# Kernel tuning notes

Measured on AMD Instinct MI355X. Metric: run time of the kernel, lower is better.

## Reference

```python
import jax, jax.numpy as jnp
import numpy as np

N, E, D, H, O = 50000, 1_600_000, 128, 64, 128
BN_EPS = 1e-5


def setup_inputs() -> dict:
    key = jax.random.key(0)
    ks = jax.random.split(key, 8)
    feat = jax.random.normal(ks[0], (N, D), dtype=jnp.float32)
    src = jax.random.randint(ks[1], (E,), 0, N, dtype=jnp.int32)
    dst = jax.random.randint(ks[2], (E,), 0, N, dtype=jnp.int32)
    s = 1.0 / np.sqrt(D)
    gamma = jnp.ones((D,), jnp.float32)
    beta = jnp.zeros((D,), jnp.float32)
    Wq = (jax.random.normal(ks[3], (D, H), dtype=jnp.float32) * s)
    bq = jnp.zeros((H,), jnp.float32)
    Wk = (jax.random.normal(ks[4], (D, H), dtype=jnp.float32) * s)
    Wv = (jax.random.normal(ks[5], (D, O), dtype=jnp.float32) * s)
    we = (jax.random.normal(ks[6], (H,), dtype=jnp.float32) / np.sqrt(H))
    return {"feat": feat, "gamma": gamma, "beta": beta, "Wq": Wq, "bq": bq,
            "Wk": Wk, "Wv": Wv, "we": we, "src": src, "dst": dst}


def reference(feat, gamma, beta, Wq, bq, Wk, Wv, we, src, dst):
    n = feat.shape[0]
    # BatchNorm1d (training-style: batch mean, biased variance)
    mean = feat.mean(axis=0)
    var = feat.var(axis=0)
    x = (feat - mean) * jax.lax.rsqrt(var + BN_EPS) * gamma + beta
    # node projections
    q = x @ Wq + bq          # [N, H]
    k = x @ Wk               # [N, H]
    v = x @ Wv               # [N, O]
    # u_add_v + fc_e(sigmoid(.)): per-edge score  [E]
    e = jax.nn.sigmoid(q[src] + k[dst]) @ we
    # edge_softmax grouped by destination node
    m = jax.ops.segment_max(e, dst, num_segments=n)
    ex = jnp.exp(e - m[dst])
    denom = jax.ops.segment_sum(ex, dst, num_segments=n)
    a = ex / denom[dst]      # [E]
    # u_mul_e_sum: weighted scatter-sum aggregation  [N, O]
    rst = jax.ops.segment_sum(v[src] * a[:, None], dst, num_segments=n)
    return rst
```

## Files before the change

### kernel.cpp

```cpp
#include <hip/hip_runtime.h>
#include <hip/hip_bf16.h>
#include <math.h>

#define BN_EPS 1e-5f
#define PGRID 256
#define CAP 96
#define CAPB 9216

typedef unsigned int u32;
typedef unsigned short u16;
typedef __attribute__((ext_vector_type(8))) short short8;
typedef __attribute__((ext_vector_type(4))) float floatx4;

__device__ __forceinline__ float bf_lo(u32 u) { return __uint_as_float(u << 16); }
__device__ __forceinline__ float bf_hi(u32 u) { return __uint_as_float(u & 0xffff0000u); }
__device__ __forceinline__ u32 bfpair(float lo, float hi) {
  u32 a = __float_as_uint(lo); a += 0x7fffu + ((a >> 16) & 1);
  u32 b = __float_as_uint(hi); b += 0x7fffu + ((b >> 16) & 1);
  return (a >> 16) | (b & 0xffff0000u);
}
__device__ __forceinline__ float sigm(float x) {
  return __builtin_amdgcn_rcpf(1.f + __expf(-x));
}

__global__ __launch_bounds__(256) void k1_stats_part_pack(
    const float* __restrict__ feat, float* __restrict__ colsum, float* __restrict__ colsq, long total,
    const int* __restrict__ src, const int* __restrict__ dst,
    int* __restrict__ bcur, u32* __restrict__ pbuf, int E, int epb, int nbuck,
    const float* __restrict__ Wq, const float* __restrict__ Wk, const float* __restrict__ Wv,
    u32* __restrict__ wt) {
  int tid = threadIdx.x;
  int bid = blockIdx.x;
  if (bid < 256) {
    long g0 = (long)bid * 256 + tid;
    float s = 0.f, sq = 0.f;
    for (long g = g0; g < total; g += 65536) { float x = feat[g]; s += x; sq += x * x; }
    __shared__ float ls[256], lq[256];
    ls[tid] = s; lq[tid] = sq;
    __syncthreads();
    if (tid < 128) {
      atomicAdd(&colsum[tid], ls[tid] + ls[tid + 128]);
      atomicAdd(&colsq[tid],  lq[tid] + lq[tid + 128]);
    }
  } else if (bid < 256 + PGRID) {
    int p = bid - 256;
    int lo = p * epb;
    int hi = lo + epb; if (hi > E) hi = E;
    __shared__ int bc_l[256], gb_l[256], cur_l[256];
    bc_l[tid] = 0;
    __syncthreads();
    for (int i = lo + tid; i < hi; i += 256)
      atomicAdd(&bc_l[dst[i] >> 8], 1);
    __syncthreads();
    if (tid < nbuck && bc_l[tid] > 0) gb_l[tid] = atomicAdd(&bcur[tid], bc_l[tid]);
    cur_l[tid] = 0;
    __syncthreads();
    for (int i = lo + tid; i < hi; i += 256) {
      int d = dst[i], s = src[i];
      int b = d >> 8;
      int r = gb_l[b] + atomicAdd(&cur_l[b], 1);
      if (r < CAPB) pbuf[(size_t)b * CAPB + r] = ((u32)(d & 255) << 16) | (u32)s;
    }
  } else {
    int col = tid;
    for (int dp = 0; dp < 64; ++dp) {
      int d = dp * 2;
      float lo, hi;
      if (col < 64)       { lo = Wq[d * 64 + col];        hi = Wq[(d + 1) * 64 + col]; }
      else if (col < 128) { lo = Wk[d * 64 + col - 64];   hi = Wk[(d + 1) * 64 + col - 64]; }
      else                { lo = Wv[d * 128 + col - 128]; hi = Wv[(d + 1) * 128 + col - 128]; }
      u32 byte = (u32)col * 256 + (u32)d * 2;
      byte ^= (u32)(col & 7) << 4;
      wt[byte >> 2] = bfpair(lo, hi);
    }
  }
}

__global__ __launch_bounds__(256) void k2_qkv_group(
    const float* __restrict__ feat, const float* __restrict__ colsum, const float* __restrict__ colsq,
    const float* __restrict__ gamma, const float* __restrict__ beta, const float* __restrict__ bq,
    const u32* __restrict__ wt,
    __hip_bfloat16* __restrict__ qbuf, float* __restrict__ kbuf, __hip_bfloat16* __restrict__ vbuf,
    int N, float invN, int QBn,
    const int* __restrict__ bcur, const u32* __restrict__ pbuf,
    int* __restrict__ cnt, u16* __restrict__ esrc) {
  int tid = threadIdx.x;
  __shared__ u32 wlds[16384];
  __shared__ float sc_lds[128], sh_lds[128];
  if ((int)blockIdx.x >= QBn) {
    int b = (int)blockIdx.x - QBn;
    int nbase = b * 256;
    int* hcur = (int*)wlds;
    hcur[tid] = 0;
    __syncthreads();
    int bc = bcur[b]; if (bc > CAPB) bc = CAPB;
    const u32* pb = pbuf + (size_t)b * CAPB;
    for (int i = tid; i < bc; i += 256) {
      u32 e = pb[i];
      int d = e >> 16, s = e & 0xffff;
      int r = atomicAdd(&hcur[d], 1);
      if (r < CAP) esrc[(size_t)(nbase + d) * CAP + r] = (u16)s;
    }
    __syncthreads();
    int nid = nbase + tid;
    if (nid < N) cnt[nid] = hcur[tid];
    return;
  }
  {
    const uint4* wg = (const uint4*)wt;
    uint4* wl = (uint4*)wlds;
#pragma unroll
    for (int i = 0; i < 16; ++i) wl[tid + i * 256] = wg[tid + i * 256];
  }
  if (tid < 128) {
    float mean = colsum[tid] * invN;
    float var  = colsq[tid] * invN - mean * mean;
    float inv  = rsqrtf(var + BN_EPS);
    float s    = gamma[tid] * inv;
    sc_lds[tid] = s; sh_lds[tid] = beta[tid] - mean * s;
  }
  __syncthreads();
  int lane = tid & 63, wv = tid >> 6;
  int arow = blockIdx.x * 64 + wv * 16 + (lane & 15);
  int kb16 = lane >> 4;
  const float* frow = feat + (long)(arow < N ? arow : N - 1) * 128;
  u32 afr[4][4];
#pragma unroll
  for (int kk = 0; kk < 4; ++kk) {
    int d0 = kk * 32 + kb16 * 8;
    float4 x0 = *(const float4*)(frow + d0);
    float4 x1 = *(const float4*)(frow + d0 + 4);
    float4 s0 = *(const float4*)&sc_lds[d0];
    float4 s1 = *(const float4*)&sc_lds[d0 + 4];
    float4 h0 = *(const float4*)&sh_lds[d0];
    float4 h1 = *(const float4*)&sh_lds[d0 + 4];
    float n0 = fmaf(x0.x, s0.x, h0.x), n1 = fmaf(x0.y, s0.y, h0.y);
    float n2 = fmaf(x0.z, s0.z, h0.z), n3 = fmaf(x0.w, s0.w, h0.w);
    float n4 = fmaf(x1.x, s1.x, h1.x), n5 = fmaf(x1.y, s1.y, h1.y);
    float n6 = fmaf(x1.z, s1.z, h1.z), n7 = fmaf(x1.w, s1.w, h1.w);
    afr[kk][0] = bfpair(n0, n1); afr[kk][1] = bfpair(n2, n3);
    afr[kk][2] = bfpair(n4, n5); afr[kk][3] = bfpair(n6, n7);
  }
  floatx4 acc[16];
#pragma unroll
  for (int ct = 0; ct < 16; ++ct) acc[ct] = (floatx4){0.f, 0.f, 0.f, 0.f};
#pragma unroll
  for (int kk = 0; kk < 4; ++kk) {
    union { u32 u[4]; short8 s; } au;
    au.u[0] = afr[kk][0]; au.u[1] = afr[kk][1]; au.u[2] = afr[kk][2]; au.u[3] = afr[kk][3];
#pragma unroll
    for (int ct = 0; ct < 16; ++ct) {
      int col = ct * 16 + (lane & 15);
      u32 byte = ((u32)col * 256 + (u32)(kk * 64 + kb16 * 16)) ^ ((u32)(col & 7) << 4);
      union { uint4 u4; short8 s; } bu;
      bu.u4 = *(const uint4*)((const char*)wlds + byte);
      acc[ct] = __builtin_amdgcn_mfma_f32_16x16x32_bf16(au.s, bu.s, acc[ct], 0, 0, 0);
    }
  }
  int crow0 = blockIdx.x * 64 + wv * 16 + (lane >> 4) * 4;
#pragma unroll
  for (int ct = 0; ct < 16; ++ct) {
    int col = ct * 16 + (lane & 15);
    float bqc = (ct < 4) ? bq[col] : 0.f;
#pragma unroll
    for (int i = 0; i < 4; ++i) {
      int row = crow0 + i;
      if (row < N) {
        float val = acc[ct][i];
        if (ct < 4)      qbuf[row * 64 + col] = __float2bfloat16(val + bqc);
        else if (ct < 8) kbuf[row * 64 + col - 64] = val;
        else             vbuf[row * 128 + col - 128] = __float2bfloat16(val);
      }
    }
  }
}

__global__ __launch_bounds__(256) void node_kernel(
    const __hip_bfloat16* __restrict__ qbt, const float* __restrict__ kb,
    const __hip_bfloat16* __restrict__ vbt, const float* __restrict__ we,
    const int* __restrict__ cnt, const u16* __restrict__ esrc,
    float* __restrict__ out, int N) {
  int tid = threadIdx.x;
  int lane = tid & 63, wvi = tid >> 6;
  int n = blockIdx.x * 4 + wvi;
  if (n >= N) return;
  int g8 = lane >> 3, hq = lane & 7;
  int deg = cnt[n]; if (deg > CAP) deg = CAP;
  int base = n * CAP;
  const uint4* qb4 = (const uint4*)qbt;
  const u32* vb32 = (const u32*)vbt;
  float4 ka  = ((const float4*)(kb + n * 64))[hq * 2];
  float4 kc  = ((const float4*)(kb + n * 64))[hq * 2 + 1];
  float4 wa  = ((const float4*)we)[hq * 2];
  float4 wb  = ((const float4*)we)[hq * 2 + 1];
  float dsum = 0.f, ax = 0.f, ay = 0.f;
  int sreg = (lane < deg) ? (int)esrc[base + lane] : 0;
  for (int cs = 0; cs < deg; cs += 64) {
    int cn = deg - cs; if (cn > 64) cn = 64;
    int rem = deg - cs - 64;
    int snext = (rem > 0 && lane < rem) ? (int)esrc[base + cs + 64 + lane] : 0;
    int nr = (cn + 7) >> 3;
    int sj0 = __shfl(sreg, g8, 64);
    uint4 qv = qb4[sj0 * 8 + hq];
    for (int r = 0; r < nr; ++r) {
      uint4 qnext;
      if (r + 1 < nr) {
        int sjn = __shfl(sreg, (r + 1) * 8 + g8, 64);
        qnext = qb4[sjn * 8 + hq];
      }
      float p;
      p  = wa.x * sigm(bf_lo(qv.x) + ka.x);
      p += wa.y * sigm(bf_hi(qv.x) + ka.y);
      p += wa.z * sigm(bf_lo(qv.y) + ka.z);
      p += wa.w * sigm(bf_hi(qv.y) + ka.w);
      p += wb.x * sigm(bf_lo(qv.z) + kc.x);
      p += wb.y * sigm(bf_hi(qv.z) + kc.y);
      p += wb.z * sigm(bf_lo(qv.w) + kc.z);
      p += wb.w * sigm(bf_hi(qv.w) + kc.w);
      p += __shfl_xor(p, 1, 64);
      p += __shfl_xor(p, 2, 64);
      p += __shfl_xor(p, 4, 64);
      int eidx = r * 8 + g8;
      float wgt = (eidx < cn) ? __expf(p) : 0.f;
      dsum += wgt;
#pragma unroll
      for (int jj = 0; jj < 8; ++jj) {
        float wj = __shfl(wgt, jj * 8, 64);
        int s2 = __shfl(sreg, r * 8 + jj, 64);
        u32 vp = vb32[s2 * 64 + lane];
        ax = fmaf(wj, bf_lo(vp), ax);
        ay = fmaf(wj, bf_hi(vp), ay);
      }
      if (r + 1 < nr) qv = qnext;
    }
    sreg = snext;
  }
  dsum += __shfl_xor(dsum, 8, 64);
  dsum += __shfl_xor(dsum, 16, 64);
  dsum += __shfl_xor(dsum, 32, 64);
  float2 r = make_float2(0.f, 0.f);
  if (deg > 0) {
    float iv = __builtin_amdgcn_rcpf(dsum);
    r.x = ax * iv; r.y = ay * iv;
  }
  ((float2*)out)[n * 64 + lane] = r;
}

extern "C" void kernel_launch(void* const* d_in, const int* in_sizes, int n_in,
                              void* d_out, int out_size, void* d_ws, size_t ws_size,
                              hipStream_t stream) {
  const float* feat  = (const float*)d_in[0];
  const float* gamma = (const float*)d_in[1];
  const float* beta  = (const float*)d_in[2];
  const float* Wq    = (const float*)d_in[3];
  const float* bq    = (const float*)d_in[4];
  const float* Wk    = (const float*)d_in[5];
  const float* Wv    = (const float*)d_in[6];
  const float* we    = (const float*)d_in[7];
  const int*   src   = (const int*)d_in[8];
  const int*   dst   = (const int*)d_in[9];
  float* out = (float*)d_out;

  const int N  = in_sizes[0] / 128;
  const int E  = in_sizes[8];
  const int QB = (N + 63) / 64;
  const int NBUCK = (N + 255) / 256;
  const int EPB = (E + PGRID - 1) / PGRID;

  char* ws = (char*)d_ws;
  size_t off = 0;
  auto alloc = [&](size_t bytes) { char* p = ws + off; off = (off + bytes + 511) & ~(size_t)511; return p; };
  float* colsum = (float*)alloc(128 * 4);
  float* colsq  = (float*)alloc(128 * 4);
  int*   bcur   = (int*)alloc((size_t)NBUCK * 4);
  u32*   wt     = (u32*)alloc(16384 * 4);
  __hip_bfloat16* qb = (__hip_bfloat16*)alloc((size_t)N * 64 * 2);
  float*          kb = (float*)alloc((size_t)N * 64 * 4);
  __hip_bfloat16* vb = (__hip_bfloat16*)alloc((size_t)N * 128 * 2);
  int* cnt  = (int*)alloc((size_t)N * 4);
  u16* esrc = (u16*)alloc((size_t)N * CAP * 2);
  u32* pbuf = (u32*)alloc((size_t)NBUCK * CAPB * 4);

  hipMemsetAsync(colsum, 0, 1024, stream);
  hipMemsetAsync(bcur, 0, (size_t)NBUCK * 4, stream);

  k1_stats_part_pack<<<256 + PGRID + 1, 256, 0, stream>>>(
      feat, colsum, colsq, (long)N * 128, src, dst, bcur, pbuf, E, EPB, NBUCK, Wq, Wk, Wv, wt);
  k2_qkv_group<<<QB + NBUCK, 256, 0, stream>>>(
      feat, colsum, colsq, gamma, beta, bq, wt, qb, kb, vb, N, 1.0f / (float)N, QB,
      bcur, pbuf, cnt, esrc);
  node_kernel<<<(N + 3) / 4, 256, 0, stream>>>(qb, kb, vb, we, cnt, esrc, out, N);
}
```

Before: 153.5 us.

## Widen partition grid, split weight packing, prescale by log2e, vectorize V gather

Doubles the edge-partition grid and spreads weight packing across 16 blocks instead of one serial block. Q and K are prescaled by log2(e) so the sigmoid uses exp2 directly. The V aggregation now loads uint2 per lane, handling two edges per half-wave, and combines the halves with a final shuffle before a float4 store. The two memsets are merged into one. Together these aim to cut a serial tail, transcendental work and memory instruction count, at the cost of some extra shuffles and slightly different bf16 rounding of the scaled Q.

```diff
diff --git a/kernel.cpp b/kernel.cpp
--- a/kernel.cpp
+++ b/kernel.cpp
@@ -3,9 +3,11 @@
 #include <math.h>
 
 #define BN_EPS 1e-5f
-#define PGRID 256
+#define PGRID 512
+#define WPACK 16
 #define CAP 96
 #define CAPB 9216
+#define LOG2E 1.4426950408889634f
 
 typedef unsigned int u32;
 typedef unsigned short u16;
@@ -19,8 +21,8 @@
   u32 b = __float_as_uint(hi); b += 0x7fffu + ((b >> 16) & 1);
   return (a >> 16) | (b & 0xffff0000u);
 }
-__device__ __forceinline__ float sigm(float x) {
-  return __builtin_amdgcn_rcpf(1.f + __expf(-x));
+__device__ __forceinline__ float sigm2(float xs) {
+  return __builtin_amdgcn_rcpf(1.f + exp2f(-xs));
 }
 
 __global__ __launch_bounds__(256) void k1_stats_part_pack(
@@ -62,8 +64,9 @@
       if (r < CAPB) pbuf[(size_t)b * CAPB + r] = ((u32)(d & 255) << 16) | (u32)s;
     }
   } else {
+    int wb = bid - (256 + PGRID);
     int col = tid;
-    for (int dp = 0; dp < 64; ++dp) {
+    for (int dp = wb * 4; dp < wb * 4 + 4; ++dp) {
       int d = dp * 2;
       float lo, hi;
       if (col < 64)       { lo = Wq[d * 64 + col];        hi = Wq[(d + 1) * 64 + col]; }
@@ -167,8 +170,8 @@
       int row = crow0 + i;
       if (row < N) {
         float val = acc[ct][i];
-        if (ct < 4)      qbuf[row * 64 + col] = __float2bfloat16(val + bqc);
-        else if (ct < 8) kbuf[row * 64 + col - 64] = val;
+        if (ct < 4)      qbuf[row * 64 + col] = __float2bfloat16((val + bqc) * LOG2E);
+        else if (ct < 8) kbuf[row * 64 + col - 64] = val * LOG2E;
         else             vbuf[row * 128 + col - 128] = __float2bfloat16(val);
       }
     }
@@ -185,15 +188,17 @@
   int n = blockIdx.x * 4 + wvi;
   if (n >= N) return;
   int g8 = lane >> 3, hq = lane & 7;
+  int l32 = lane & 31, ehalf = lane >> 5;
   int deg = cnt[n]; if (deg > CAP) deg = CAP;
   int base = n * CAP;
   const uint4* qb4 = (const uint4*)qbt;
-  const u32* vb32 = (const u32*)vbt;
+  const uint2* vb2 = (const uint2*)vbt;
   float4 ka  = ((const float4*)(kb + n * 64))[hq * 2];
   float4 kc  = ((const float4*)(kb + n * 64))[hq * 2 + 1];
   float4 wa  = ((const float4*)we)[hq * 2];
   float4 wb  = ((const float4*)we)[hq * 2 + 1];
-  float dsum = 0.f, ax = 0.f, ay = 0.f;
+  float dsum = 0.f;
+  float a0 = 0.f, a1 = 0.f, a2 = 0.f, a3 = 0.f;
   int sreg = (lane < deg) ? (int)esrc[base + lane] : 0;
   for (int cs = 0; cs < deg; cs += 64) {
     int cn = deg - cs; if (cn > 64) cn = 64;
@@ -209,27 +214,30 @@
         qnext = qb4[sjn * 8 + hq];
       }
       float p;
-      p  = wa.x * sigm(bf_lo(qv.x) + ka.x);
-      p += wa.y * sigm(bf_hi(qv.x) + ka.y);
-      p += wa.z * sigm(bf_lo(qv.y) + ka.z);
-      p += wa.w * sigm(bf_hi(qv.y) + ka.w);
-      p += wb.x * sigm(bf_lo(qv.z) + kc.x);
-      p += wb.y * sigm(bf_hi(qv.z) + kc.y);
-      p += wb.z * sigm(bf_lo(qv.w) + kc.z);
-      p += wb.w * sigm(bf_hi(qv.w) + kc.w);
+      p  = wa.x * sigm2(bf_lo(qv.x) + ka.x);
+      p += wa.y * sigm2(bf_hi(qv.x) + ka.y);
+      p += wa.z * sigm2(bf_lo(qv.y) + ka.z);
+      p += wa.w * sigm2(bf_hi(qv.y) + ka.w);
+      p += wb.x * sigm2(bf_lo(qv.z) + kc.x);
+      p += wb.y * sigm2(bf_hi(qv.z) + kc.y);
+      p += wb.z * sigm2(bf_lo(qv.w) + kc.z);
+      p += wb.w * sigm2(bf_hi(qv.w) + kc.w);
       p += __shfl_xor(p, 1, 64);
       p += __shfl_xor(p, 2, 64);
       p += __shfl_xor(p, 4, 64);
       int eidx = r * 8 + g8;
-      float wgt = (eidx < cn) ? __expf(p) : 0.f;
+      float wgt = (eidx < cn) ? exp2f(p * LOG2E) : 0.f;
       dsum += wgt;
 #pragma unroll
-      for (int jj = 0; jj < 8; ++jj) {
-        float wj = __shfl(wgt, jj * 8, 64);
-        int s2 = __shfl(sreg, r * 8 + jj, 64);
-        u32 vp = vb32[s2 * 64 + lane];
-        ax = fmaf(wj, bf_lo(vp), ax);
-        ay = fmaf(wj, bf_hi(vp), ay);
+      for (int pp = 0; pp < 4; ++pp) {
+        int le = pp * 2 + ehalf;
+        float wj = __shfl(wgt, le * 8, 64);
+        int s2   = __shfl(sreg, r * 8 + le, 64);
+        uint2 vp = vb2[s2 * 32 + l32];
+        a0 = fmaf(wj, bf_lo(vp.x), a0);
+        a1 = fmaf(wj, bf_hi(vp.x), a1);
+        a2 = fmaf(wj, bf_lo(vp.y), a2);
+        a3 = fmaf(wj, bf_hi(vp.y), a3);
       }
       if (r + 1 < nr) qv = qnext;
     }
@@ -238,12 +246,18 @@
   dsum += __shfl_xor(dsum, 8, 64);
   dsum += __shfl_xor(dsum, 16, 64);
   dsum += __shfl_xor(dsum, 32, 64);
-  float2 r = make_float2(0.f, 0.f);
-  if (deg > 0) {
-    float iv = __builtin_amdgcn_rcpf(dsum);
-    r.x = ax * iv; r.y = ay * iv;
-  }
-  ((float2*)out)[n * 64 + lane] = r;
+  a0 += __shfl_xor(a0, 32, 64);
+  a1 += __shfl_xor(a1, 32, 64);
+  a2 += __shfl_xor(a2, 32, 64);
+  a3 += __shfl_xor(a3, 32, 64);
+  if (lane < 32) {
+    float4 o = make_float4(0.f, 0.f, 0.f, 0.f);
+    if (deg > 0) {
+      float iv = __builtin_amdgcn_rcpf(dsum);
+      o = make_float4(a0 * iv, a1 * iv, a2 * iv, a3 * iv);
+    }
+    ((float4*)out)[n * 32 + l32] = o;
+  }
 }
 
 extern "C" void kernel_launch(void* const* d_in, const int* in_sizes, int n_in,
@@ -270,9 +284,9 @@
   char* ws = (char*)d_ws;
   size_t off = 0;
   auto alloc = [&](size_t bytes) { char* p = ws + off; off = (off + bytes + 511) & ~(size_t)511; return p; };
-  float* colsum = (float*)alloc(128 * 4);
-  float* colsq  = (float*)alloc(128 * 4);
-  int*   bcur   = (int*)alloc((size_t)NBUCK * 4);
+  float* colsum = (float*)alloc(2048);
+  float* colsq  = colsum + 128;
+  int*   bcur   = (int*)(colsum + 256);
   u32*   wt     = (u32*)alloc(16384 * 4);
   __hip_bfloat16* qb = (__hip_bfloat16*)alloc((size_t)N * 64 * 2);
   float*          kb = (float*)alloc((size_t)N * 64 * 4);
@@ -281,10 +295,9 @@
   u16* esrc = (u16*)alloc((size_t)N * CAP * 2);
   u32* pbuf = (u32*)alloc((size_t)NBUCK * CAPB * 4);
 
-  hipMemsetAsync(colsum, 0, 1024, stream);
-  hipMemsetAsync(bcur, 0, (size_t)NBUCK * 4, stream);
-
-  k1_stats_part_pack<<<256 + PGRID + 1, 256, 0, stream>>>(
+  hipMemsetAsync(colsum, 0, 2048, stream);
+
+  k1_stats_part_pack<<<256 + PGRID + WPACK, 256, 0, stream>>>(
       feat, colsum, colsq, (long)N * 128, src, dst, bcur, pbuf, E, EPB, NBUCK, Wq, Wk, Wv, wt);
   k2_qkv_group<<<QB + NBUCK, 256, 0, stream>>>(
       feat, colsum, colsq, gamma, beta, bq, wt, qb, kb, vb, N, 1.0f / (float)N, QB,
```

Result: no change. 153.3 us (-0.1%).
